# Kernel tuning notes

Hardware: AMD Instinct MI355X
Metric: run time of the kernel (lower is better)

The kernel has to match this reference:

```python
import jax, jax.numpy as jnp
import numpy as np

BIG = 1e10  # sentinel for invalid pairwise distances


def get_xyz(depth, fx, fy, cx, cy):
    # depth: [B,1,H,W] -> xyz: [B,3,H,W] via pinhole unprojection
    B, _, H, W = depth.shape
    v = jnp.arange(H, dtype=depth.dtype)[:, None]   # rows
    u = jnp.arange(W, dtype=depth.dtype)[None, :]   # cols
    z = depth[:, 0]                                  # [B,H,W]
    x = (u - cx) / fx * z
    y = (v - cy) / fy * z
    return jnp.stack([x, y, z], axis=1)              # [B,3,H,W]


def _chamfer_item(p, g, vp, vg):
    # p,g: [N,3] point sets; vp,vg: [N] bool validity masks
    # squared pairwise distances via ||p||^2 + ||g||^2 - 2 p.g
    d = (jnp.sum(p * p, -1)[:, None] + jnp.sum(g * g, -1)[None, :]
         - 2.0 * (p @ g.T))                          # [N,N]
    d = jnp.maximum(d, 0.0)
    has_g = jnp.any(vg)
    has_p = jnp.any(vp)
    d1 = jnp.min(jnp.where(vg[None, :], d, BIG), axis=1)  # per pred point
    d2 = jnp.min(jnp.where(vp[:, None], d, BIG), axis=0)  # per gt point
    s1 = jnp.sum(jnp.where(vp & has_g, d1, 0.0))
    s2 = jnp.sum(jnp.where(vg & has_p, d2, 0.0))
    return s1 + s2


def reference(pred, gt_xyz, mask, fx, fy, cx, cy):
    B = pred.shape[0]
    pred_xyz = get_xyz(pred, fx, fy, cx, cy)             # [B,3,H,W]
    p = pred_xyz.reshape(B, 3, -1).transpose(0, 2, 1)    # [B,N,3]
    g = gt_xyz.reshape(B, 3, -1).transpose(0, 2, 1)      # [B,N,3]
    m = mask[:, 0].reshape(B, -1) > 0                    # [B,N]
    # ignore_zeros=True: drop points whose coordinate sum is exactly 0
    vp = m & (jnp.sum(p, -1) != 0)
    vg = m & (jnp.sum(g, -1) != 0)
    per_item = jax.vmap(_chamfer_item)(p, g, vp, vg)     # [B]
    return jnp.sum(per_item) / B


def setup_inputs() -> dict:
    key = jax.random.key(0)
    k1, k2, k3 = jax.random.split(key, 3)
    B, H, W = 2, 128, 128
    pred = jax.random.uniform(k1, (B, 1, H, W), dtype=jnp.float32) * 2.0 + 0.1
    gt_xyz = jax.random.normal(k2, (B, 3, H, W), dtype=jnp.float32)
    mask = jax.random.randint(k3, (B, 1, H, W), 0, 2, dtype=jnp.int32)
    fx = jnp.float32(525.0)
    fy = jnp.float32(525.0)
    cx = jnp.float32(64.0)
    cy = jnp.float32(64.0)
    return {"pred": pred, "gt_xyz": gt_xyz, "mask": mask,
            "fx": fx, "fy": fy, "cx": cx, "cy": cy}
```

## Files before the change

### kernel.cpp

```cpp
#include <hip/hip_runtime.h>

#define B_ITEMS 2
#define W_IMG   128
#define N_PTS   16384
#define CH_GRID 1024

__global__ __launch_bounds__(256) void prep_kernel(
        const float* __restrict__ pred,
        const float* __restrict__ gt,
        const int*   __restrict__ mask,
        const float* fxp, const float* fyp,
        const float* cxp, const float* cyp,
        int*    __restrict__ cnt,
        float4* __restrict__ pR, float4* __restrict__ gR,
        float4* __restrict__ pT, float4* __restrict__ gT,
        float*  __restrict__ out) {
    int s    = blockIdx.x >> 6;
    int b    = s & 1;
    int isG  = s >> 1;
    int tid  = threadIdx.x;
    int idx  = (blockIdx.x & 63) * 256 + tid;
    int lane = tid & 63, w = tid >> 6;

    if (blockIdx.x == 0 && tid == 0) out[0] = 0.0f;

    float x, y, z;
    if (!isG) {
        float fx = *fxp, fy = *fyp, cx = *cxp, cy = *cyp;
        float u = (float)(idx & (W_IMG - 1));
        float v = (float)(idx >> 7);
        z = pred[b * N_PTS + idx];
        x = (u - cx) / fx * z;
        y = (v - cy) / fy * z;
    } else {
        x = gt[(b * 3 + 0) * N_PTS + idx];
        y = gt[(b * 3 + 1) * N_PTS + idx];
        z = gt[(b * 3 + 2) * N_PTS + idx];
    }
    int  mv = mask[b * N_PTS + idx];
    bool ok = (mv > 0) && (((x + y) + z) != 0.0f);

    unsigned long long bal = __ballot(ok);
    int nw  = __popcll(bal);
    int pre = __popcll(bal & ((1ull << lane) - 1ull));

    __shared__ int wbase[4];
    __shared__ int blockbase;
    if (lane == 0) wbase[w] = nw;
    __syncthreads();
    if (tid == 0) {
        int s0 = 0;
#pragma unroll
        for (int i = 0; i < 4; ++i) { int t = wbase[i]; wbase[i] = s0; s0 += t; }
        blockbase = s0 ? atomicAdd(&cnt[s], s0) : 0;
    }
    __syncthreads();

    if (ok) {
        int pos = blockbase + wbase[w] + pre;
        float ps = fmaf(z, z, fmaf(y, y, x * x));
        float4* __restrict__ raw = (isG ? gR : pR) + b * N_PTS;
        float4* __restrict__ tf  = (isG ? gT : pT) + b * N_PTS;
        raw[pos] = make_float4(x, y, z, ps);
        tf[pos]  = make_float4(-2.0f * x, -2.0f * y, -2.0f * z, ps);
    }
}

__global__ __launch_bounds__(256, 4) void chamfer_kernel(
        const int*    __restrict__ cnt,
        const float4* __restrict__ pR, const float4* __restrict__ gR,
        const float4* __restrict__ pT, const float4* __restrict__ gT,
        float* __restrict__ out) {
    int np0 = cnt[0], np1 = cnt[1], ng0 = cnt[2], ng1 = cnt[3];
    int naArr[4] = {np0, ng0, np1, ng1};
    int nbArr[4] = {ng0, np0, ng1, np1};
    const float4* Arow[4] = {pR, gR, pR + N_PTS, gR + N_PTS};
    const float4* Bcol[4] = {gT, pT, gT + N_PTS, pT + N_PTS};

    int units[4];
    int Utot = 0;
#pragma unroll
    for (int i = 0; i < 4; ++i) {
        units[i] = (naArr[i] > 0 && nbArr[i] > 0) ? ((naArr[i] + 63) >> 6) : 0;
        Utot += units[i];
    }
    int u = blockIdx.x;
    if (u >= Utot) return;
    int s = 0;
    while (u >= units[s]) { u -= units[s]; ++s; }
    int na = naArr[s], nb = nbArr[s];
    const float4* __restrict__ A  = Arow[s];
    const float4* __restrict__ Bp = Bcol[s];
    int rowbase = u * 64;

    int tid = threadIdx.x;
    int tr = tid & 7, tc = tid >> 3;

    float px[8], py[8], pz[8], rm[8];
#pragma unroll
    for (int a = 0; a < 8; ++a) {
        float4 v = A[rowbase + a * 8 + tr];
        px[a] = v.x; py[a] = v.y; pz[a] = v.z;
        rm[a] = 3.4e38f;
    }

    int full = nb >> 8;
    float4 bufA[8], bufB[8];
    auto LOADT = [&](float4* buf, int t) {
#pragma unroll
        for (int cb = 0; cb < 8; ++cb)
            buf[cb] = Bp[t * 256 + cb * 32 + tc];
    };
    auto COMPT = [&](const float4* buf) {
#pragma unroll
        for (int cb = 0; cb < 8; ++cb) {
            float bx = buf[cb].x, by = buf[cb].y, bz = buf[cb].z, bw = buf[cb].w;
#pragma unroll
            for (int a = 0; a < 8; ++a) {
                float t = fmaf(px[a], bx, fmaf(py[a], by, fmaf(pz[a], bz, bw)));
                rm[a] = fminf(rm[a], t);
            }
        }
    };

    if (full > 0) {
        LOADT(bufA, 0);
        int t = 0;
        for (; t + 2 <= full; t += 2) {
            LOADT(bufB, t + 1);
            COMPT(bufA);
            if (t + 2 < full) LOADT(bufA, t + 2);
            COMPT(bufB);
        }
        if (t < full) COMPT(bufA);
    }

    if (nb & 255) {
        int t = full;
#pragma unroll
        for (int cb = 0; cb < 8; ++cb) {
            int j = t * 256 + cb * 32 + tc;
            float4 v = Bp[j];
            bool okc = j < nb;
            float bx = okc ? v.x : 0.0f;
            float by = okc ? v.y : 0.0f;
            float bz = okc ? v.z : 0.0f;
            float bw = okc ? v.w : 3.4e38f;
#pragma unroll
            for (int a = 0; a < 8; ++a) {
                float tv = fmaf(px[a], bx, fmaf(py[a], by, fmaf(pz[a], bz, bw)));
                rm[a] = fminf(rm[a], tv);
            }
        }
    }

#pragma unroll
    for (int a = 0; a < 8; ++a) {
        float v = rm[a];
        v = fminf(v, __shfl_xor(v, 8, 64));
        v = fminf(v, __shfl_xor(v, 16, 64));
        v = fminf(v, __shfl_xor(v, 32, 64));
        rm[a] = v;
    }
    __shared__ float smin[4][64];
    int w = tid >> 6, lane = tid & 63;
    if (lane < 8) {
#pragma unroll
        for (int a = 0; a < 8; ++a) smin[w][a * 8 + lane] = rm[a];
    }
    __syncthreads();
    if (tid < 64) {
        float v = fminf(fminf(smin[0][tid], smin[1][tid]),
                        fminf(smin[2][tid], smin[3][tid]));
        int row = rowbase + tid;
        float ps = A[row].w;
        float contrib = (row < na) ? fmaxf(v + ps, 0.0f) : 0.0f;
#pragma unroll
        for (int off = 32; off > 0; off >>= 1)
            contrib += __shfl_down(contrib, off, 64);
        if (tid == 0) atomicAdd(out, contrib * (1.0f / B_ITEMS));
    }
}

extern "C" void kernel_launch(void* const* d_in, const int* in_sizes, int n_in,
                              void* d_out, int out_size, void* d_ws, size_t ws_size,
                              hipStream_t stream) {
    const float* pred = (const float*)d_in[0];
    const float* gt   = (const float*)d_in[1];
    const int*   mask = (const int*)  d_in[2];
    const float* fx   = (const float*)d_in[3];
    const float* fy   = (const float*)d_in[4];
    const float* cx   = (const float*)d_in[5];
    const float* cy   = (const float*)d_in[6];
    float* out = (float*)d_out;

    char* ws = (char*)d_ws;
    size_t SEG = (size_t)B_ITEMS * N_PTS * 16;
    int*    cnt = (int*)ws;
    float4* pR  = (float4*)(ws + 256);
    float4* gR  = (float4*)(ws + 256 + SEG);
    float4* pT  = (float4*)(ws + 256 + 2 * SEG);
    float4* gT  = (float4*)(ws + 256 + 3 * SEG);

    hipMemsetAsync(cnt, 0, 16, stream);

    prep_kernel<<<dim3(256), 256, 0, stream>>>(
        pred, gt, mask, fx, fy, cx, cy, cnt, pR, gR, pT, gT, out);

    chamfer_kernel<<<dim3(CH_GRID), 256, 0, stream>>>(
        cnt, pR, gR, pT, gT, out);
}
```

Measured before the change: 115.4 us.

## Shrink chamfer row tile to 32 rows with 4 rows per thread

Each chamfer block now covers 32 rows instead of 64. Each thread handles 4 rows instead of 8, with 32 column lanes per row group, and the grid doubles to 2048 blocks. The occupancy hint is raised to 6 blocks per SM, and the final cross-lane min reduction is simplified to a single 32-row shared array. The aim is to cut register pressure and raise occupancy and block count so the ~16K-row workload spreads across more CUs. The trade-off is that arithmetic intensity per column load is halved, so B columns are re-read from cache twice as often, and the explicit double-buffer prefetch is dropped.

```diff
diff --git a/kernel.cpp b/kernel.cpp
--- a/kernel.cpp
+++ b/kernel.cpp
@@ -3,7 +3,7 @@
 #define B_ITEMS 2
 #define W_IMG   128
 #define N_PTS   16384
-#define CH_GRID 1024
+#define CH_GRID 2048
 
 __global__ __launch_bounds__(256) void prep_kernel(
         const float* __restrict__ pred,
@@ -66,7 +66,15 @@
     }
 }
 
-__global__ __launch_bounds__(256, 4) void chamfer_kernel(
+#define COMP4(c)                                                              \
+    do {                                                                      \
+        rm0 = fminf(rm0, fmaf(px0, (c).x, fmaf(py0, (c).y, fmaf(pz0, (c).z, (c).w)))); \
+        rm1 = fminf(rm1, fmaf(px1, (c).x, fmaf(py1, (c).y, fmaf(pz1, (c).z, (c).w)))); \
+        rm2 = fminf(rm2, fmaf(px2, (c).x, fmaf(py2, (c).y, fmaf(pz2, (c).z, (c).w)))); \
+        rm3 = fminf(rm3, fmaf(px3, (c).x, fmaf(py3, (c).y, fmaf(pz3, (c).z, (c).w)))); \
+    } while (0)
+
+__global__ __launch_bounds__(256, 6) void chamfer_kernel(
         const int*    __restrict__ cnt,
         const float4* __restrict__ pR, const float4* __restrict__ gR,
         const float4* __restrict__ pT, const float4* __restrict__ gT,
@@ -81,7 +89,7 @@
     int Utot = 0;
 #pragma unroll
     for (int i = 0; i < 4; ++i) {
-        units[i] = (naArr[i] > 0 && nbArr[i] > 0) ? ((naArr[i] + 63) >> 6) : 0;
+        units[i] = (naArr[i] > 0 && nbArr[i] > 0) ? ((naArr[i] + 31) >> 5) : 0;
         Utot += units[i];
     }
     int u = blockIdx.x;
@@ -91,93 +99,74 @@
     int na = naArr[s], nb = nbArr[s];
     const float4* __restrict__ A  = Arow[s];
     const float4* __restrict__ Bp = Bcol[s];
-    int rowbase = u * 64;
+    int rowbase = u * 32;
 
     int tid = threadIdx.x;
-    int tr = tid & 7, tc = tid >> 3;
-
-    float px[8], py[8], pz[8], rm[8];
-#pragma unroll
-    for (int a = 0; a < 8; ++a) {
-        float4 v = A[rowbase + a * 8 + tr];
-        px[a] = v.x; py[a] = v.y; pz[a] = v.z;
-        rm[a] = 3.4e38f;
-    }
-
-    int full = nb >> 8;
-    float4 bufA[8], bufB[8];
-    auto LOADT = [&](float4* buf, int t) {
-#pragma unroll
-        for (int cb = 0; cb < 8; ++cb)
-            buf[cb] = Bp[t * 256 + cb * 32 + tc];
-    };
-    auto COMPT = [&](const float4* buf) {
-#pragma unroll
-        for (int cb = 0; cb < 8; ++cb) {
-            float bx = buf[cb].x, by = buf[cb].y, bz = buf[cb].z, bw = buf[cb].w;
-#pragma unroll
-            for (int a = 0; a < 8; ++a) {
-                float t = fmaf(px[a], bx, fmaf(py[a], by, fmaf(pz[a], bz, bw)));
-                rm[a] = fminf(rm[a], t);
-            }
+    int tc = tid & 31, tr = tid >> 5;
+
+    float4 r0 = A[rowbase +  0 + tr];
+    float4 r1 = A[rowbase +  8 + tr];
+    float4 r2 = A[rowbase + 16 + tr];
+    float4 r3 = A[rowbase + 24 + tr];
+    float px0 = r0.x, py0 = r0.y, pz0 = r0.z;
+    float px1 = r1.x, py1 = r1.y, pz1 = r1.z;
+    float px2 = r2.x, py2 = r2.y, pz2 = r2.z;
+    float px3 = r3.x, py3 = r3.y, pz3 = r3.z;
+    float rm0 = 3.4e38f, rm1 = 3.4e38f, rm2 = 3.4e38f, rm3 = 3.4e38f;
+
+    int full = nb >> 7;
+    int t = 0;
+    for (; t + 2 <= full; t += 2) {
+        const float4* __restrict__ bp = Bp + t * 128 + tc;
+        float4 u0 = bp[0],   u1 = bp[32],  u2 = bp[64],  u3 = bp[96];
+        float4 v0 = bp[128], v1 = bp[160], v2 = bp[192], v3 = bp[224];
+        COMP4(u0); COMP4(u1); COMP4(u2); COMP4(u3);
+        COMP4(v0); COMP4(v1); COMP4(v2); COMP4(v3);
+    }
+    if (t < full) {
+        const float4* __restrict__ bp = Bp + t * 128 + tc;
+        float4 u0 = bp[0], u1 = bp[32], u2 = bp[64], u3 = bp[96];
+        COMP4(u0); COMP4(u1); COMP4(u2); COMP4(u3);
+    }
+    if (nb & 127) {
+        int jb = full * 128 + tc;
+#pragma unroll
+        for (int q = 0; q < 4; ++q) {
+            int j = jb + q * 32;
+            float4 v = Bp[j];
+            float4 c;
+            bool okc = j < nb;
+            c.x = okc ? v.x : 0.0f;
+            c.y = okc ? v.y : 0.0f;
+            c.z = okc ? v.z : 0.0f;
+            c.w = okc ? v.w : 3.4e38f;
+            COMP4(c);
         }
-    };
-
-    if (full > 0) {
-        LOADT(bufA, 0);
-        int t = 0;
-        for (; t + 2 <= full; t += 2) {
-            LOADT(bufB, t + 1);
-            COMPT(bufA);
-            if (t + 2 < full) LOADT(bufA, t + 2);
-            COMPT(bufB);
-        }
-        if (t < full) COMPT(bufA);
-    }
-
-    if (nb & 255) {
-        int t = full;
-#pragma unroll
-        for (int cb = 0; cb < 8; ++cb) {
-            int j = t * 256 + cb * 32 + tc;
-            float4 v = Bp[j];
-            bool okc = j < nb;
-            float bx = okc ? v.x : 0.0f;
-            float by = okc ? v.y : 0.0f;
-            float bz = okc ? v.z : 0.0f;
-            float bw = okc ? v.w : 3.4e38f;
-#pragma unroll
-            for (int a = 0; a < 8; ++a) {
-                float tv = fmaf(px[a], bx, fmaf(py[a], by, fmaf(pz[a], bz, bw)));
-                rm[a] = fminf(rm[a], tv);
-            }
-        }
-    }
-
-#pragma unroll
-    for (int a = 0; a < 8; ++a) {
-        float v = rm[a];
-        v = fminf(v, __shfl_xor(v, 8, 64));
-        v = fminf(v, __shfl_xor(v, 16, 64));
-        v = fminf(v, __shfl_xor(v, 32, 64));
-        rm[a] = v;
-    }
-    __shared__ float smin[4][64];
-    int w = tid >> 6, lane = tid & 63;
-    if (lane < 8) {
-#pragma unroll
-        for (int a = 0; a < 8; ++a) smin[w][a * 8 + lane] = rm[a];
+    }
+
+#pragma unroll
+    for (int off = 1; off <= 16; off <<= 1) {
+        rm0 = fminf(rm0, __shfl_xor(rm0, off, 64));
+        rm1 = fminf(rm1, __shfl_xor(rm1, off, 64));
+        rm2 = fminf(rm2, __shfl_xor(rm2, off, 64));
+        rm3 = fminf(rm3, __shfl_xor(rm3, off, 64));
+    }
+    __shared__ float smin[32];
+    if (tc == 0) {
+        smin[ 0 + tr] = rm0;
+        smin[ 8 + tr] = rm1;
+        smin[16 + tr] = rm2;
+        smin[24 + tr] = rm3;
     }
     __syncthreads();
-    if (tid < 64) {
-        float v = fminf(fminf(smin[0][tid], smin[1][tid]),
-                        fminf(smin[2][tid], smin[3][tid]));
+    if (tid < 32) {
         int row = rowbase + tid;
+        float v  = smin[tid];
         float ps = A[row].w;
         float contrib = (row < na) ? fmaxf(v + ps, 0.0f) : 0.0f;
 #pragma unroll
-        for (int off = 32; off > 0; off >>= 1)
-            contrib += __shfl_down(contrib, off, 64);
+        for (int off = 16; off > 0; off >>= 1)
+            contrib += __shfl_down(contrib, off, 32);
         if (tid == 0) atomicAdd(out, contrib * (1.0f / B_ITEMS));
     }
 }
```

After: 116.3 us. No clear change (+0.8%).

## Stage B-column tiles in double-buffered shared memory and remap thread tiling

Applied to the files above, without the earlier changes.

Each block now loads every 256-point column tile once, cooperatively, into a double-buffered LDS array instead of having each thread fetch eight float4s per tile from global/L1. The thread mapping changes so that 32 threads share a row group and 8 row groups cover the 64 rows, which means the per-row min is now reduced across 32 lanes within a wavefront. Out-of-range entries are padded on load, so the separate tail loop goes away. The cost is a __syncthreads per tile and LDS traffic. The old version relied on cache reuse of redundant global loads across 8 lanes.

```diff
diff --git a/kernel.cpp b/kernel.cpp
--- a/kernel.cpp
+++ b/kernel.cpp
@@ -94,7 +94,7 @@
     int rowbase = u * 64;
 
     int tid = threadIdx.x;
-    int tr = tid & 7, tc = tid >> 3;
+    int tc = tid & 31, tr = tid >> 5;
 
     float px[8], py[8], pz[8], rm[8];
 #pragma unroll
@@ -104,75 +104,66 @@
         rm[a] = 3.4e38f;
     }
 
-    int full = nb >> 8;
-    float4 bufA[8], bufB[8];
-    auto LOADT = [&](float4* buf, int t) {
-#pragma unroll
-        for (int cb = 0; cb < 8; ++cb)
-            buf[cb] = Bp[t * 256 + cb * 32 + tc];
-    };
-    auto COMPT = [&](const float4* buf) {
+    __shared__ float4 sB[2][256];
+    __shared__ float  smin[64];
+    int ntiles = (nb + 255) >> 8;
+
+    {
+        int j = tid;
+        float4 v = Bp[min(j, N_PTS - 1)];
+        bool okc = j < nb;
+        float4 r;
+        r.x = okc ? v.x : 0.0f;
+        r.y = okc ? v.y : 0.0f;
+        r.z = okc ? v.z : 0.0f;
+        r.w = okc ? v.w : 3.4e38f;
+        sB[0][tid] = r;
+    }
+    __syncthreads();
+
+    for (int t = 0; t < ntiles; ++t) {
+        float4 r;
+        bool have = (t + 1 < ntiles);
+        if (have) {
+            int j = (t + 1) * 256 + tid;
+            float4 v = Bp[min(j, N_PTS - 1)];
+            bool okc = j < nb;
+            r.x = okc ? v.x : 0.0f;
+            r.y = okc ? v.y : 0.0f;
+            r.z = okc ? v.z : 0.0f;
+            r.w = okc ? v.w : 3.4e38f;
+        }
+        const float4* __restrict__ buf = sB[t & 1];
 #pragma unroll
         for (int cb = 0; cb < 8; ++cb) {
-            float bx = buf[cb].x, by = buf[cb].y, bz = buf[cb].z, bw = buf[cb].w;
-#pragma unroll
-            for (int a = 0; a < 8; ++a) {
-                float t = fmaf(px[a], bx, fmaf(py[a], by, fmaf(pz[a], bz, bw)));
-                rm[a] = fminf(rm[a], t);
-            }
+            float4 c = buf[cb * 32 + tc];
+#pragma unroll
+            for (int a = 0; a < 8; ++a)
+                rm[a] = fminf(rm[a],
+                    fmaf(px[a], c.x, fmaf(py[a], c.y, fmaf(pz[a], c.z, c.w))));
         }
-    };
-
-    if (full > 0) {
-        LOADT(bufA, 0);
-        int t = 0;
-        for (; t + 2 <= full; t += 2) {
-            LOADT(bufB, t + 1);
-            COMPT(bufA);
-            if (t + 2 < full) LOADT(bufA, t + 2);
-            COMPT(bufB);
-        }
-        if (t < full) COMPT(bufA);
-    }
-
-    if (nb & 255) {
-        int t = full;
-#pragma unroll
-        for (int cb = 0; cb < 8; ++cb) {
-            int j = t * 256 + cb * 32 + tc;
-            float4 v = Bp[j];
-            bool okc = j < nb;
-            float bx = okc ? v.x : 0.0f;
-            float by = okc ? v.y : 0.0f;
-            float bz = okc ? v.z : 0.0f;
-            float bw = okc ? v.w : 3.4e38f;
-#pragma unroll
-            for (int a = 0; a < 8; ++a) {
-                float tv = fmaf(px[a], bx, fmaf(py[a], by, fmaf(pz[a], bz, bw)));
-                rm[a] = fminf(rm[a], tv);
-            }
-        }
+        if (have) sB[(t + 1) & 1][tid] = r;
+        __syncthreads();
     }
 
 #pragma unroll
     for (int a = 0; a < 8; ++a) {
         float v = rm[a];
+        v = fminf(v, __shfl_xor(v, 1, 64));
+        v = fminf(v, __shfl_xor(v, 2, 64));
+        v = fminf(v, __shfl_xor(v, 4, 64));
         v = fminf(v, __shfl_xor(v, 8, 64));
         v = fminf(v, __shfl_xor(v, 16, 64));
-        v = fminf(v, __shfl_xor(v, 32, 64));
         rm[a] = v;
     }
-    __shared__ float smin[4][64];
-    int w = tid >> 6, lane = tid & 63;
-    if (lane < 8) {
-#pragma unroll
-        for (int a = 0; a < 8; ++a) smin[w][a * 8 + lane] = rm[a];
+    if (tc == 0) {
+#pragma unroll
+        for (int a = 0; a < 8; ++a) smin[a * 8 + tr] = rm[a];
     }
     __syncthreads();
     if (tid < 64) {
-        float v = fminf(fminf(smin[0][tid], smin[1][tid]),
-                        fminf(smin[2][tid], smin[3][tid]));
         int row = rowbase + tid;
+        float v  = smin[tid];
         float ps = A[row].w;
         float contrib = (row < na) ? fmaxf(v + ps, 0.0f) : 0.0f;
 #pragma unroll
```

Measured after the change: 104.2 us. -9.7%, faster.
